# Performance work log

Hardware: AMD Instinct MI355X
Metric: run time of the kernel (lower is better)

Reference implementation:

```python
import jax, jax.numpy as jnp
import numpy as np

N, B, S, A = 4, 32768, 512, 64
H = 256          # hidden_size
NH = 16          # effective number of heads = attend_dim (range(attend_dim) bug in source)
D = 16           # attend_dim = hidden // attend_heads
EPS_BN = 1e-5


def setup_inputs() -> dict:
    key = jax.random.key(0)
    ks = jax.random.split(key, 16)
    sc = 0.05
    return {
        "states": jax.random.normal(ks[0], (N, B, S), dtype=jnp.float32),
        "actions": jax.random.normal(ks[1], (N, B, A), dtype=jnp.float32),
        # per-agent state+action encoder (enc_fc1)
        "Wenc": jax.random.normal(ks[2], (N, S + A, H), dtype=jnp.float32) * sc,
        "benc": jax.random.normal(ks[3], (N, H), dtype=jnp.float32) * sc,
        # per-agent state encoder (s_enc_fc1)
        "Ws": jax.random.normal(ks[4], (N, S, H), dtype=jnp.float32) * sc,
        "bs": jax.random.normal(ks[5], (N, H), dtype=jnp.float32) * sc,
        # shared per-head extractors (no bias on key/selector; bias on value)
        "Wk": jax.random.normal(ks[6], (NH, H, D), dtype=jnp.float32) * sc,
        "Wsel": jax.random.normal(ks[7], (NH, H, D), dtype=jnp.float32) * sc,
        "Wv": jax.random.normal(ks[8], (NH, H, D), dtype=jnp.float32) * sc,
        "bv": jax.random.normal(ks[9], (NH, D), dtype=jnp.float32) * sc,
        # per-agent critic MLP (input = H + NH*D = 2H)
        "Wc1": jax.random.normal(ks[10], (N, 2 * H, H), dtype=jnp.float32) * sc,
        "bc1": jax.random.normal(ks[11], (N, H), dtype=jnp.float32) * sc,
        "Wc2": jax.random.normal(ks[12], (N, H, A), dtype=jnp.float32) * sc,
        "bc2": jax.random.normal(ks[13], (N, A), dtype=jnp.float32) * sc,
    }


def _lrelu(x):
    return jax.nn.leaky_relu(x, 0.01)


def _bn(x):
    # BatchNorm1d(affine=False), training mode: biased batch stats over batch axis
    m = x.mean(axis=1, keepdims=True)
    v = x.var(axis=1, keepdims=True)
    return (x - m) * jax.lax.rsqrt(v + EPS_BN)


def reference(states, actions, Wenc, benc, Ws, bs, Wk, Wsel, Wv, bv, Wc1, bc1, Wc2, bc2):
    n, b = states.shape[0], states.shape[1]
    # state+action encodings per agent: [n, B, H]
    sa = jnp.concatenate([states, actions], axis=-1)
    sa_enc = _lrelu(jnp.einsum('nbi,nih->nbh', _bn(sa), Wenc) + benc[:, None, :])
    # state encodings per agent: [n, B, H]
    s_enc = _lrelu(jnp.einsum('nbs,nsh->nbh', _bn(states), Ws) + bs[:, None, :])
    # per-head keys/values/selectors: [NH, n, B, D]
    keys = jnp.einsum('nbh,ehd->enbd', sa_enc, Wk)
    vals = _lrelu(jnp.einsum('nbh,ehd->enbd', sa_enc, Wv) + bv[:, None, None, :])
    sel = jnp.einsum('nbh,ehd->enbd', s_enc, Wsel)
    # attention of agent i over agents j != i (self excluded via -inf mask)
    logits = jnp.einsum('eibd,ejbd->eibj', sel, keys) / jnp.sqrt(jnp.float32(D))
    self_mask = jnp.eye(n, dtype=bool)[None, :, None, :]  # [1, i, 1, j]
    probs = jax.nn.softmax(jnp.where(self_mask, -1e9, logits), axis=-1)
    # weighted values: [n, B, NH, D] (head-major concat order)
    other = jnp.einsum('eibj,ejbd->ibed', probs, vals)
    critic_in = jnp.concatenate([s_enc, other.reshape(n, b, NH * D)], axis=-1)  # [n, B, 2H]
    h = _lrelu(jnp.einsum('nbc,nch->nbh', critic_in, Wc1) + bc1[:, None, :])
    all_q = jnp.einsum('nbh,nha->nba', h, Wc2) + bc2[:, None, :]  # [n, B, A]
    idx = jnp.argmax(actions, axis=-1)  # [n, B]
    q = jnp.take_along_axis(all_q, idx[..., None], axis=-1)  # [n, B, 1]
    return q
```

## Files before the change

kernel.cpp:

```cpp
#include <hip/hip_runtime.h>
#include <hip/hip_bf16.h>
#include <cstdint>
#include <cstddef>

using bf16 = __hip_bfloat16;
typedef __attribute__((ext_vector_type(8))) short bf16x8v;
typedef __attribute__((ext_vector_type(4))) float f32x4v;

constexpr int Nn = 4;
constexpr int Bb = 32768;
constexpr int Ss = 512;
constexpr int Av = 64;
constexpr int SA = 576;
constexpr float BN_EPS = 1e-5f;

__device__ __forceinline__ float lrelu(float v){ return v >= 0.f ? v : 0.01f * v; }
__device__ __forceinline__ float bf2f(bf16 x){ return __bfloat162float(x); }
__device__ __forceinline__ short f2bf(float v){
  union { bf16 b; short s; } u; u.b = __float2bfloat16(v); return u.s;
}

__global__ __launch_bounds__(256) void bn_stats(const float* __restrict__ states,
                                                const float* __restrict__ actions,
                                                float* __restrict__ ssum,
                                                float* __restrict__ ssq){
  const int n = blockIdx.z;
  const int f = blockIdx.x * 64 + threadIdx.x;
  const int ty = threadIdx.y;
  const float* p; int step;
  if (f < Ss){ p = states  + (size_t)n*Bb*Ss + f;        step = Ss; }
  else       { p = actions + (size_t)n*Bb*Av + (f - Ss); step = Av; }
  float s = 0.f, q = 0.f;
  const int b0 = blockIdx.y * 512 + ty, bend = blockIdx.y * 512 + 512;
  for (int b = b0; b < bend; b += 4){
    float v = p[(size_t)b * step];
    s += v; q += v * v;
  }
  __shared__ float rs[4][64], rq[4][64];
  rs[ty][threadIdx.x] = s; rq[ty][threadIdx.x] = q;
  __syncthreads();
  if (ty == 0){
    s = rs[0][threadIdx.x] + rs[1][threadIdx.x] + rs[2][threadIdx.x] + rs[3][threadIdx.x];
    q = rq[0][threadIdx.x] + rq[1][threadIdx.x] + rq[2][threadIdx.x] + rq[3][threadIdx.x];
    atomicAdd(&ssum[n*SA + f], s);
    atomicAdd(&ssq [n*SA + f], q);
  }
}

__global__ void bn_finalize(const float* __restrict__ ssum, const float* __restrict__ ssq,
                            float* __restrict__ mean, float* __restrict__ rstd){
  int i = blockIdx.x * 256 + threadIdx.x;
  float m = ssum[i] * (1.f / Bb);
  float v = ssq[i] * (1.f / Bb) - m * m;
  v = fmaxf(v, 0.f);
  mean[i] = m;
  rstd[i] = rsqrtf(v + BN_EPS);
}

__global__ void bias_copy(const float* __restrict__ b1, const float* __restrict__ b2,
                          float* __restrict__ o1, float* __restrict__ o2){
  int i = blockIdx.x * 256 + threadIdx.x;
  if (i < Nn*256){ o1[i] = b1[i]; o2[i] = b2[i]; }
}

template<int HEAD>
__global__ __launch_bounds__(256) void foldT2(const float* __restrict__ src,
                                              const float* __restrict__ scale,
                                              const float* __restrict__ mean,
                                              float* __restrict__ bias_out,
                                              short* __restrict__ dst,
                                              int K, int N){
  const int a  = blockIdx.z;
  const int tx = threadIdx.x & 63;
  const int ty = threadIdx.x >> 6;
  const int f0 = blockIdx.x * 64 + ty * 16;
  const int c  = blockIdx.y * 64 + tx;
  const float* s = src + (HEAD ? 0 : (size_t)a*K*N);
  short tmp[16] __attribute__((aligned(16)));
  float bsum = 0.f;
  #pragma unroll
  for (int j = 0; j < 16; j++){
    const int f = f0 + j;
    float w = HEAD ? s[(((size_t)(c >> 4))*K + f)*16 + (c & 15)]
                   : s[(size_t)f*N + c];
    if (scale) w *= scale[a*SA + f];
    if (mean)  bsum += mean[a*SA + f] * w;
    tmp[j] = f2bf(w);
  }
  short* d = dst + (HEAD ? 0 : (size_t)a*K*N) + (size_t)c*K + f0;
  *(bf16x8v*)d       = *(bf16x8v*)tmp;
  *(bf16x8v*)(d + 8) = *(bf16x8v*)(tmp + 8);
  if (mean){
    __shared__ float red[4][64];
    red[ty][tx] = bsum;
    __syncthreads();
    if (threadIdx.x < 64){
      float t = red[0][threadIdx.x] + red[1][threadIdx.x]
              + red[2][threadIdx.x] + red[3][threadIdx.x];
      atomicAdd(&bias_out[a*N + blockIdx.y*64 + threadIdx.x], -t);
    }
  }
}

template<int BM,int BN,int WM,int WN,int K,int ASRC,bool ACT,bool OUTF32>
__global__ __launch_bounds__(256) void mgemm(const void* A1, const void* A2,
                                             const short* __restrict__ Wp, int wPerAgent,
                                             const float* __restrict__ bias, int biasStride,
                                             void* Out, int outPitch){
  __shared__ __align__(16) short As[BM*40];
  __shared__ __align__(16) short Bs[BN*40];
  const int tid  = threadIdx.x;
  const int a    = blockIdx.z;
  const int row0 = blockIdx.x * BM;
  const int col0 = blockIdx.y * BN;
  const short* Wb = Wp + (size_t)a * wPerAgent;
  constexpr int FM = BM/WM/16, FN = BN/WN/16;
  const int wid = tid >> 6, lane = tid & 63;
  const int wm = wid % WM, wn = wid / WM;
  const int rowB = wm*(BM/WM), colB = wn*(BN/WN);
  const int lrow = lane & 15, lq = lane >> 4;

  f32x4v acc[FM][FN];
  #pragma unroll
  for (int i = 0; i < FM; i++)
    #pragma unroll
    for (int j = 0; j < FN; j++) acc[i][j] = (f32x4v){0.f,0.f,0.f,0.f};

  for (int k0 = 0; k0 < K; k0 += 32){
    {
      constexpr int EA = BM/8;
      int r, kq;
      if constexpr (BM == 128){ r = tid >> 1; kq = (tid & 1)*16; }
      else                    { r = tid >> 2; kq = (tid & 3)*8;  }
      const size_t grow = (size_t)a*Bb + row0 + r;
      #pragma unroll
      for (int c8 = 0; c8 < EA; c8 += 8){
        const int f = k0 + kq + c8;
        if constexpr (ASRC == 0 || ASRC == 1){
          const float* sp;
          if constexpr (ASRC == 0)
            sp = (f < 512) ? (const float*)A1 + grow*512 + f
                           : (const float*)A2 + grow*64 + (f - 512);
          else
            sp = (const float*)A1 + grow*512 + f;
          float4 x0 = *(const float4*)sp;
          float4 x1 = *(const float4*)(sp + 4);
          short tmp[8] = { f2bf(x0.x), f2bf(x0.y), f2bf(x0.z), f2bf(x0.w),
                           f2bf(x1.x), f2bf(x1.y), f2bf(x1.z), f2bf(x1.w) };
          *(bf16x8v*)&As[r*40 + kq + c8] = *(bf16x8v*)tmp;
        } else {
          const short* sp;
          if constexpr (ASRC == 3)
            sp = (f < 256) ? (const short*)A1 + grow*256 + f
                           : (const short*)A2 + grow*256 + (f - 256);
          else
            sp = (const short*)A1 + grow*256 + f;
          *(bf16x8v*)&As[r*40 + kq + c8] = *(const bf16x8v*)sp;
        }
      }
    }
    {
      int n, kq, reps;
      if constexpr      (BN == 256){ n = tid;      kq = 0;            reps = 4; }
      else if constexpr (BN == 128){ n = tid >> 1; kq = (tid & 1)*16; reps = 2; }
      else                         { n = tid >> 2; kq = (tid & 3)*8;  reps = 1; }
      const short* wp = Wb + (size_t)(col0 + n)*K + k0 + kq;
      #pragma unroll
      for (int t = 0; t < reps; t++)
        *(bf16x8v*)&Bs[n*40 + kq + t*8] = *(const bf16x8v*)(wp + t*8);
    }
    __syncthreads();
    bf16x8v af[FM], bfr[FN];
    #pragma unroll
    for (int mi = 0; mi < FM; mi++)
      af[mi] = *(const bf16x8v*)&As[(rowB + mi*16 + lrow)*40 + lq*8];
    #pragma unroll
    for (int ni = 0; ni < FN; ni++)
      bfr[ni] = *(const bf16x8v*)&Bs[(colB + ni*16 + lrow)*40 + lq*8];
    #pragma unroll
    for (int mi = 0; mi < FM; mi++)
      #pragma unroll
      for (int ni = 0; ni < FN; ni++)
        acc[mi][ni] = __builtin_amdgcn_mfma_f32_16x16x32_bf16(af[mi], bfr[ni], acc[mi][ni], 0, 0, 0);
    __syncthreads();
  }
  #pragma unroll
  for (int mi = 0; mi < FM; mi++){
    const size_t gr = (size_t)a*Bb + row0 + rowB + mi*16 + lq*4;
    #pragma unroll
    for (int ni = 0; ni < FN; ni++){
      const int gc = col0 + colB + ni*16 + lrow;
      const float bb = bias ? bias[a*biasStride + gc] : 0.f;
      #pragma unroll
      for (int r = 0; r < 4; r++){
        float v = acc[mi][ni][r] + bb;
        if (ACT) v = lrelu(v);
        if constexpr (OUTF32) ((float*)Out)[(gr + r)*(size_t)outPitch + gc] = v;
        else                  ((bf16*) Out)[(gr + r)*(size_t)outPitch + gc] = __float2bfloat16(v);
      }
    }
  }
}

union B8g { uint4 u; bf16 h[8]; };
__global__ __launch_bounds__(256) void attn_g(const bf16* __restrict__ K_,
                                              const bf16* __restrict__ V_,
                                              bf16* SO){
  const int t = blockIdx.x * 256 + threadIdx.x;
  const int e = t & 15;
  const size_t b = t >> 4;
  const size_t ofs = b*256 + e*16;
  float S[4][16], Kf[4][16], Vf[4][16];
  #pragma unroll
  for (int i = 0; i < 4; i++){
    B8g u0, u1;
    const bf16* sp = SO + (size_t)i*Bb*256 + ofs;
    u0.u = *(const uint4*)sp; u1.u = *(const uint4*)(sp + 8);
    #pragma unroll
    for (int l = 0; l < 8; l++){ S[i][l] = bf2f(u0.h[l]); S[i][8+l] = bf2f(u1.h[l]); }
    const bf16* kp = K_ + (size_t)i*Bb*256 + ofs;
    u0.u = *(const uint4*)kp; u1.u = *(const uint4*)(kp + 8);
    #pragma unroll
    for (int l = 0; l < 8; l++){ Kf[i][l] = bf2f(u0.h[l]); Kf[i][8+l] = bf2f(u1.h[l]); }
    const bf16* vp = V_ + (size_t)i*Bb*256 + ofs;
    u0.u = *(const uint4*)vp; u1.u = *(const uint4*)(vp + 8);
    #pragma unroll
    for (int l = 0; l < 8; l++){ Vf[i][l] = bf2f(u0.h[l]); Vf[i][8+l] = bf2f(u1.h[l]); }
  }
  #pragma unroll
  for (int i = 0; i < 4; i++){
    float lg[4];
    #pragma unroll
    for (int j = 0; j < 4; j++){
      float d = 0.f;
      #pragma unroll
      for (int l = 0; l < 16; l++) d += S[i][l] * Kf[j][l];
      lg[j] = d * 0.25f;
    }
    lg[i] = -1e9f;
    float m = fmaxf(fmaxf(lg[0], lg[1]), fmaxf(lg[2], lg[3]));
    float p[4], s = 0.f;
    #pragma unroll
    for (int j = 0; j < 4; j++){ p[j] = expf(lg[j] - m); s += p[j]; }
    p[i] = 0.f;
    const float inv = 1.f / s;
    float o[16] = {};
    #pragma unroll
    for (int j = 0; j < 4; j++){
      const float pj = p[j] * inv;
      #pragma unroll
      for (int l = 0; l < 16; l++) o[l] += pj * Vf[j][l];
    }
    B8g w0, w1;
    #pragma unroll
    for (int l = 0; l < 8; l++){ w0.h[l] = __float2bfloat16(o[l]); w1.h[l] = __float2bfloat16(o[8+l]); }
    bf16* op = SO + (size_t)i*Bb*256 + ofs;
    *(uint4*)op       = w0.u;
    *(uint4*)(op + 8) = w1.u;
  }
}

__global__ __launch_bounds__(256) void sel_q(const float* __restrict__ actions,
                                             const float* __restrict__ allq,
                                             float* __restrict__ out){
  const size_t i = (size_t)blockIdx.x * 256 + threadIdx.x;
  const float* ap = actions + i*64;
  float best = ap[0]; int bi = 0;
  for (int j = 1; j < 64; j++){
    float v = ap[j];
    if (v > best){ best = v; bi = j; }
  }
  out[i] = allq[i*64 + bi];
}

constexpr int RB = 4;

template<int K>
__device__ __forceinline__ void gemm4_glb(const float* __restrict__ st,
                                          const float* __restrict__ ac,
                                          const float* __restrict__ mean,
                                          const float* __restrict__ rstd,
                                          int a, int brow0, int tid,
                                          const float* __restrict__ W,
                                          const float* __restrict__ bias, bool act,
                                          float (*Xs)[68], float (*Wt)[264],
                                          float (*Sout)[256]){
  const int r = tid >> 6, c4 = (tid & 63) * 4;
  float acc[4] = {};
  for (int k0 = 0; k0 < K; k0 += 8){
    if (tid < 32){
      const int rb = tid >> 3, kq = tid & 7;
      const int f = k0 + kq;
      float v = (f < Ss) ? st[((size_t)a*Bb + brow0 + rb)*Ss + f]
                         : ac[((size_t)a*Bb + brow0 + rb)*Av + (f - Ss)];
      Xs[kq][rb] = (v - mean[a*SA + f]) * rstd[a*SA + f];
    }
    {
      const int wk = tid >> 5, wc = (tid & 31) * 8;
      const float* wp = W + (size_t)(k0 + wk) * 256 + wc;
      *(float4*)&Wt[wk][wc]     = *(const float4*)wp;
      *(float4*)&Wt[wk][wc + 4] = *(const float4*)(wp + 4);
    }
    __syncthreads();
    #pragma unroll
    for (int kk = 0; kk < 8; kk++){
      const float av = Xs[kk][r];
      float4 w = *(const float4*)&Wt[kk][c4];
      acc[0] += av*w.x; acc[1] += av*w.y; acc[2] += av*w.z; acc[3] += av*w.w;
    }
    __syncthreads();
  }
  float4 o;
  o.x = acc[0] + (bias ? bias[c4+0] : 0.f);
  o.y = acc[1] + (bias ? bias[c4+1] : 0.f);
  o.z = acc[2] + (bias ? bias[c4+2] : 0.f);
  o.w = acc[3] + (bias ? bias[c4+3] : 0.f);
  if (act){ o.x = lrelu(o.x); o.y = lrelu(o.y); o.z = lrelu(o.z); o.w = lrelu(o.w); }
  *(float4*)&Sout[a*RB + r][c4] = o;
}

template<int K, bool HEAD>
__device__ __forceinline__ void gemm4_lds(const float (*S1)[256], const float (*S2)[256],
                                          int a, int tid,
                                          const float* __restrict__ W,
                                          const float* __restrict__ bias, bool act,
                                          float (*Wt)[264], float (*Sout)[256]){
  const int r = tid >> 6, c4 = (tid & 63) * 4;
  float acc[4] = {};
  for (int k0 = 0; k0 < K; k0 += 8){
    if (HEAD){
      const int wk = tid >> 5, c8 = (tid & 31) * 8;
      const int e = c8 >> 4, d0 = c8 & 15;
      const float* wp = W + (size_t)e*(256*16) + (size_t)(k0 + wk)*16 + d0;
      *(float4*)&Wt[wk][c8]     = *(const float4*)wp;
      *(float4*)&Wt[wk][c8 + 4] = *(const float4*)(wp + 4);
    } else {
      const int wk = tid >> 5, wc = (tid & 31) * 8;
      const float* wp = W + (size_t)(k0 + wk)*256 + wc;
      *(float4*)&Wt[wk][wc]     = *(const float4*)wp;
      *(float4*)&Wt[wk][wc + 4] = *(const float4*)(wp + 4);
    }
    __syncthreads();
    const float (*src)[256] = (k0 < 256) ? S1 : S2;
    const int kb = (k0 < 256) ? k0 : k0 - 256;
    const float* arow = &src[a*RB + r][kb];
    #pragma unroll
    for (int kk = 0; kk < 8; kk++){
      const float av = arow[kk];
      float4 w = *(const float4*)&Wt[kk][c4];
      acc[0] += av*w.x; acc[1] += av*w.y; acc[2] += av*w.z; acc[3] += av*w.w;
    }
    __syncthreads();
  }
  float4 o;
  o.x = acc[0] + (bias ? bias[c4+0] : 0.f);
  o.y = acc[1] + (bias ? bias[c4+1] : 0.f);
  o.z = acc[2] + (bias ? bias[c4+2] : 0.f);
  o.w = acc[3] + (bias ? bias[c4+3] : 0.f);
  if (act){ o.x = lrelu(o.x); o.y = lrelu(o.y); o.z = lrelu(o.z); o.w = lrelu(o.w); }
  *(float4*)&Sout[a*RB + r][c4] = o;
}

__global__ __launch_bounds__(256) void fused(
    const float* __restrict__ states, const float* __restrict__ actions,
    const float* __restrict__ mean,  const float* __restrict__ rstd,
    const float* __restrict__ Wenc, const float* __restrict__ benc,
    const float* __restrict__ Wsx,  const float* __restrict__ bsx,
    const float* __restrict__ Wk,   const float* __restrict__ Wsel,
    const float* __restrict__ Wv,   const float* __restrict__ bv,
    const float* __restrict__ Wc1,  const float* __restrict__ bc1,
    const float* __restrict__ Wc2,  const float* __restrict__ bc2,
    float* __restrict__ qout){
  __shared__ float A [16][256];
  __shared__ float Bs2[16][256];
  __shared__ float C [16][256];
  __shared__ float Wt[8][264];
  __shared__ float Xs[8][68];
  __shared__ float Cq[4][68];
  const int tid   = threadIdx.x;
  const int brow0 = blockIdx.x * RB;
  for (int a = 0; a < Nn; a++)
    gemm4_glb<Ss>(states, actions, mean, rstd, a, brow0, tid,
                  Wsx + (size_t)a*Ss*256, bsx + a*256, true, Xs, Wt, A);
  __syncthreads();
  for (int a = 0; a < Nn; a++)
    gemm4_lds<256, true>(A, nullptr, a, tid, Wsel, nullptr, false, Wt, C);
  __syncthreads();
  for (int a = 0; a < Nn; a++)
    gemm4_glb<SA>(states, actions, mean, rstd, a, brow0, tid,
                  Wenc + (size_t)a*SA*256, benc + a*256, true, Xs, Wt, A);
  __syncthreads();
  for (int a = 0; a < Nn; a++)
    gemm4_lds<256, true>(A, nullptr, a, tid, Wk, nullptr, false, Wt, Bs2);
  __syncthreads();
  for (int a = 0; a < Nn; a++)
    gemm4_lds<256, true>(A, nullptr, a, tid, Wv, bv, true, Wt, A);
  __syncthreads();
  if (tid < 64){
    const int rb = tid >> 4, e = tid & 15;
    const int co = e * 16;
    float S[4][16], Kf[4][16], Vf[4][16];
    #pragma unroll
    for (int i = 0; i < 4; i++)
      #pragma unroll
      for (int l = 0; l < 16; l++){
        S[i][l]  = C  [i*RB + rb][co + l];
        Kf[i][l] = Bs2[i*RB + rb][co + l];
        Vf[i][l] = A  [i*RB + rb][co + l];
      }
    #pragma unroll
    for (int i = 0; i < 4; i++){
      float lg[4];
      #pragma unroll
      for (int j = 0; j < 4; j++){
        float d = 0.f;
        #pragma unroll
        for (int l = 0; l < 16; l++) d += S[i][l] * Kf[j][l];
        lg[j] = d * 0.25f;
      }
      lg[i] = -1e9f;
      float m = fmaxf(fmaxf(lg[0], lg[1]), fmaxf(lg[2], lg[3]));
      float p[4], s = 0.f;
      #pragma unroll
      for (int j = 0; j < 4; j++){ p[j] = expf(lg[j] - m); s += p[j]; }
      p[i] = 0.f;
      const float inv = 1.f / s;
      float o[16] = {};
      #pragma unroll
      for (int j = 0; j < 4; j++){
        const float pj = p[j] * inv;
        #pragma unroll
        for (int l = 0; l < 16; l++) o[l] += pj * Vf[j][l];
      }
      #pragma unroll
      for (int l = 0; l < 16; l++) C[i*RB + rb][co + l] = o[l];
    }
  }
  __syncthreads();
  for (int a = 0; a < Nn; a++)
    gemm4_glb<Ss>(states, actions, mean, rstd, a, brow0, tid,
                  Wsx + (size_t)a*Ss*256, bsx + a*256, true, Xs, Wt, A);
  __syncthreads();
  for (int a = 0; a < Nn; a++)
    gemm4_lds<512, false>(A, C, a, tid, Wc1 + (size_t)a*512*256, bc1 + a*256, true, Wt, Bs2);
  __syncthreads();
  for (int a = 0; a < Nn; a++){
    const int r2 = tid >> 6, c2 = tid & 63;
    float acc = 0.f;
    for (int k0 = 0; k0 < 256; k0 += 8){
      const int wk = tid >> 5, wc = (tid & 31) * 2;
      const float* wp = Wc2 + (size_t)a*256*64 + (size_t)(k0 + wk)*64 + wc;
      Wt[wk][wc]     = wp[0];
      Wt[wk][wc + 1] = wp[1];
      __syncthreads();
      #pragma unroll
      for (int kk = 0; kk < 8; kk++) acc += Bs2[a*RB + r2][k0 + kk] * Wt[kk][c2];
      __syncthreads();
    }
    Cq[r2][c2] = acc + bc2[a*64 + c2];
    __syncthreads();
    if (tid < RB){
      const float* ap = actions + ((size_t)a*Bb + brow0 + tid)*Av;
      float best = ap[0]; int bi = 0;
      for (int j = 1; j < Av; j++){
        float v = ap[j];
        if (v > best){ best = v; bi = j; }
      }
      qout[(size_t)a*Bb + brow0 + tid] = Cq[tid][bi];
    }
    __syncthreads();
  }
}

extern "C" void kernel_launch(void* const* d_in, const int* in_sizes, int n_in,
                              void* d_out, int out_size, void* d_ws, size_t ws_size,
                              hipStream_t stream){
  (void)in_sizes; (void)n_in; (void)out_size;
  const float* states  = (const float*)d_in[0];
  const float* actions = (const float*)d_in[1];
  const float* Wenc    = (const float*)d_in[2];
  const float* benc    = (const float*)d_in[3];
  const float* Wsx     = (const float*)d_in[4];
  const float* bsx     = (const float*)d_in[5];
  const float* Wk      = (const float*)d_in[6];
  const float* Wsel    = (const float*)d_in[7];
  const float* Wv      = (const float*)d_in[8];
  const float* bv      = (const float*)d_in[9];
  const float* Wc1     = (const float*)d_in[10];
  const float* bc1     = (const float*)d_in[11];
  const float* Wc2     = (const float*)d_in[12];
  const float* bc2     = (const float*)d_in[13];
  float* qout = (float*)d_out;

  char* base = (char*)d_ws;
  float* ssum = (float*)base;
  float* ssq  = ssum + Nn*SA;
  float* mean = ssq  + Nn*SA;
  float* rstd = mean + Nn*SA;
  size_t off = 4*Nn*SA*sizeof(float);
  float* benc_p = (float*)(base + off); off += 4096;
  float* bs_p   = (float*)(base + off); off += 4096;
  short* Wenc_p = (short*)(base + off); off += (size_t)Nn*SA*256*2;
  short* Ws_p   = (short*)(base + off); off += (size_t)Nn*Ss*256*2;
  short* Whk_p  = (short*)(base + off); off += 256*256*2;
  short* Whs_p  = (short*)(base + off); off += 256*256*2;
  short* Whv_p  = (short*)(base + off); off += 256*256*2;
  short* Wc1_p  = (short*)(base + off); off += (size_t)Nn*512*256*2;
  short* Wc2_p  = (short*)(base + off); off += (size_t)Nn*64*256*2;
  const size_t BUFB = (size_t)Nn*Bb*256*2;
  bf16* S   = (bf16*)(base + off); off += BUFB;
  bf16* SEL = (bf16*)(base + off); off += BUFB;
  bf16* E   = (bf16*)(base + off); off += BUFB;
  bf16* KB  = (bf16*)(base + off); off += BUFB;
  const size_t need = off;
  float* ALLQ = (float*)E;

  hipMemsetAsync(ssum, 0, 2*Nn*SA*sizeof(float), stream);
  bn_stats<<<dim3(9, 64, Nn), dim3(64, 4), 0, stream>>>(states, actions, ssum, ssq);
  bn_finalize<<<dim3(9), dim3(256), 0, stream>>>(ssum, ssq, mean, rstd);

  if (ws_size >= need){
    bias_copy<<<dim3(4), 256, 0, stream>>>(benc, bsx, benc_p, bs_p);
    foldT2<0><<<dim3(SA/64, 4, Nn), 256, 0, stream>>>(Wenc, rstd, mean, benc_p, Wenc_p, SA, 256);
    foldT2<0><<<dim3(Ss/64, 4, Nn), 256, 0, stream>>>(Wsx,  rstd, mean, bs_p,   Ws_p,  Ss, 256);
    foldT2<1><<<dim3(4, 4, 1), 256, 0, stream>>>(Wk,   nullptr, nullptr, nullptr, Whk_p, 256, 256);
    foldT2<1><<<dim3(4, 4, 1), 256, 0, stream>>>(Wsel, nullptr, nullptr, nullptr, Whs_p, 256, 256);
    foldT2<1><<<dim3(4, 4, 1), 256, 0, stream>>>(Wv,   nullptr, nullptr, nullptr, Whv_p, 256, 256);
    foldT2<0><<<dim3(8, 4, Nn), 256, 0, stream>>>(Wc1, nullptr, nullptr, nullptr, Wc1_p, 512, 256);
    foldT2<0><<<dim3(4, 1, Nn), 256, 0, stream>>>(Wc2, nullptr, nullptr, nullptr, Wc2_p, 256, 64);

    mgemm<128,128,2,2,576,0,true,false><<<dim3(Bb/128, 2, Nn), 256, 0, stream>>>(
        states, actions, Wenc_p, SA*256, benc_p, 256, E, 256);
    mgemm<128,128,2,2,512,1,true,false><<<dim3(Bb/128, 2, Nn), 256, 0, stream>>>(
        states, nullptr, Ws_p, Ss*256, bs_p, 256, S, 256);
    mgemm<128,128,2,2,256,2,false,false><<<dim3(Bb/128, 2, Nn), 256, 0, stream>>>(
        S, nullptr, Whs_p, 0, nullptr, 0, SEL, 256);
    mgemm<128,128,2,2,256,2,false,false><<<dim3(Bb/128, 2, Nn), 256, 0, stream>>>(
        E, nullptr, Whk_p, 0, nullptr, 0, KB, 256);
    mgemm<64,256,1,4,256,2,true,false><<<dim3(Bb/64, 1, Nn), 256, 0, stream>>>(
        E, nullptr, Whv_p, 0, bv, 0, E, 256);
    attn_g<<<dim3(Bb*16/256), 256, 0, stream>>>(KB, E, SEL);
    mgemm<128,128,2,2,512,3,true,false><<<dim3(Bb/128, 2, Nn), 256, 0, stream>>>(
        S, SEL, Wc1_p, 512*256, bc1, 256, KB, 256);
    mgemm<128,64,2,2,256,2,false,true><<<dim3(Bb/128, 1, Nn), 256, 0, stream>>>(
        KB, nullptr, Wc2_p, 64*256, bc2, 64, ALLQ, 64);
    sel_q<<<dim3(Nn*Bb/256), 256, 0, stream>>>(actions, ALLQ, qout);
  } else {
    fused<<<dim3(Bb/RB), 256, 0, stream>>>(states, actions, mean, rstd,
                                           Wenc, benc, Wsx, bsx,
                                           Wk, Wsel, Wv, bv,
                                           Wc1, bc1, Wc2, bc2, qout);
  }
}
```

Baseline: 1.016 ms.

## Fuse bf16 input conversion into BN stats pass and retile GEMMs to 64x256

The batch-norm statistics kernel now reads four features per thread with float4 loads and also writes a bf16 copy of the concatenated states and actions into a workspace buffer. The two encoder GEMMs then read that bf16 buffer instead of re-reading and converting the fp32 inputs twice, and most GEMMs switch from 128x128 to 64x256 tiles. The SEL and KB buffers are aliased onto the Xbf region, which is only safe because Xbf is dead by the time they are written. The trade-off is an extra bf16 write of the inputs in exchange for halving fp32 input reads and the repeated conversion work.

New measurement: 1.046 ms. 3.0% more time.

```diff
diff --git a/kernel.cpp b/kernel.cpp
--- a/kernel.cpp
+++ b/kernel.cpp
@@ -5,6 +5,7 @@
 
 using bf16 = __hip_bfloat16;
 typedef __attribute__((ext_vector_type(8))) short bf16x8v;
+typedef __attribute__((ext_vector_type(4))) short bf16x4v;
 typedef __attribute__((ext_vector_type(4))) float f32x4v;
 
 constexpr int Nn = 4;
@@ -20,30 +21,51 @@
   union { bf16 b; short s; } u; u.b = __float2bfloat16(v); return u.s;
 }
 
-__global__ __launch_bounds__(256) void bn_stats(const float* __restrict__ states,
-                                                const float* __restrict__ actions,
-                                                float* __restrict__ ssum,
-                                                float* __restrict__ ssq){
-  const int n = blockIdx.z;
-  const int f = blockIdx.x * 64 + threadIdx.x;
+template<bool WRX>
+__global__ __launch_bounds__(256) void conv_stats(const float* __restrict__ states,
+                                                  const float* __restrict__ actions,
+                                                  float* __restrict__ ssum,
+                                                  float* __restrict__ ssq,
+                                                  short* __restrict__ Xbf){
+  const int n  = blockIdx.z;
+  const int tx = threadIdx.x;
   const int ty = threadIdx.y;
-  const float* p; int step;
-  if (f < Ss){ p = states  + (size_t)n*Bb*Ss + f;        step = Ss; }
-  else       { p = actions + (size_t)n*Bb*Av + (f - Ss); step = Av; }
-  float s = 0.f, q = 0.f;
+  const int g  = blockIdx.x * 64 + tx;
+  const bool on = g < (SA / 4);
+  const int f  = g * 4;
+  const float* p = nullptr; int step = 0;
+  if (on){
+    if (f < Ss){ p = states  + (size_t)n*Bb*Ss + f;        step = Ss; }
+    else       { p = actions + (size_t)n*Bb*Av + (f - Ss); step = Av; }
+  }
+  float s0=0.f,s1=0.f,s2=0.f,s3=0.f,q0=0.f,q1=0.f,q2=0.f,q3=0.f;
   const int b0 = blockIdx.y * 512 + ty, bend = blockIdx.y * 512 + 512;
-  for (int b = b0; b < bend; b += 4){
-    float v = p[(size_t)b * step];
-    s += v; q += v * v;
-  }
-  __shared__ float rs[4][64], rq[4][64];
-  rs[ty][threadIdx.x] = s; rq[ty][threadIdx.x] = q;
-  __syncthreads();
-  if (ty == 0){
-    s = rs[0][threadIdx.x] + rs[1][threadIdx.x] + rs[2][threadIdx.x] + rs[3][threadIdx.x];
-    q = rq[0][threadIdx.x] + rq[1][threadIdx.x] + rq[2][threadIdx.x] + rq[3][threadIdx.x];
-    atomicAdd(&ssum[n*SA + f], s);
-    atomicAdd(&ssq [n*SA + f], q);
+  if (on){
+    for (int b = b0; b < bend; b += 4){
+      float4 v = *(const float4*)(p + (size_t)b*step);
+      if (WRX){
+        short t4[4] __attribute__((aligned(8))) =
+            { f2bf(v.x), f2bf(v.y), f2bf(v.z), f2bf(v.w) };
+        *(bf16x4v*)&Xbf[((size_t)n*Bb + b)*SA + f] = *(bf16x4v*)t4;
+      }
+      s0 += v.x; q0 += v.x*v.x;
+      s1 += v.y; q1 += v.y*v.y;
+      s2 += v.z; q2 += v.z*v.z;
+      s3 += v.w; q3 += v.w*v.w;
+    }
+  }
+  __shared__ float rs[4][64][4], rq[4][64][4];
+  rs[ty][tx][0]=s0; rs[ty][tx][1]=s1; rs[ty][tx][2]=s2; rs[ty][tx][3]=s3;
+  rq[ty][tx][0]=q0; rq[ty][tx][1]=q1; rq[ty][tx][2]=q2; rq[ty][tx][3]=q3;
+  __syncthreads();
+  if (ty == 0 && on){
+    #pragma unroll
+    for (int j = 0; j < 4; j++){
+      float ts = rs[0][tx][j]+rs[1][tx][j]+rs[2][tx][j]+rs[3][tx][j];
+      float tq = rq[0][tx][j]+rq[1][tx][j]+rq[2][tx][j]+rq[3][tx][j];
+      atomicAdd(&ssum[n*SA + f + j], ts);
+      atomicAdd(&ssq [n*SA + f + j], tq);
+    }
   }
 }
 
@@ -102,7 +124,7 @@
   }
 }
 
-template<int BM,int BN,int WM,int WN,int K,int ASRC,bool ACT,bool OUTF32>
+template<int BM,int BN,int WM,int WN,int K,int ASRC,int AP,bool ACT,bool OUTF32>
 __global__ __launch_bounds__(256) void mgemm(const void* A1, const void* A2,
                                              const short* __restrict__ Wp, int wPerAgent,
                                              const float* __restrict__ bias, int biasStride,
@@ -154,7 +176,7 @@
             sp = (f < 256) ? (const short*)A1 + grow*256 + f
                            : (const short*)A2 + grow*256 + (f - 256);
           else
-            sp = (const short*)A1 + grow*256 + f;
+            sp = (const short*)A1 + grow*(size_t)AP + f;
           *(bf16x8v*)&As[r*40 + kq + c8] = *(const bf16x8v*)sp;
         }
       }
@@ -508,18 +530,22 @@
   short* Wc1_p  = (short*)(base + off); off += (size_t)Nn*512*256*2;
   short* Wc2_p  = (short*)(base + off); off += (size_t)Nn*64*256*2;
   const size_t BUFB = (size_t)Nn*Bb*256*2;
-  bf16* S   = (bf16*)(base + off); off += BUFB;
-  bf16* SEL = (bf16*)(base + off); off += BUFB;
-  bf16* E   = (bf16*)(base + off); off += BUFB;
-  bf16* KB  = (bf16*)(base + off); off += BUFB;
+  const size_t XBFB = (size_t)Nn*Bb*SA*2;
+  short* Xbf = (short*)(base + off);
+  bf16* SEL  = (bf16*)(base + off);
+  bf16* KB   = (bf16*)(base + off + BUFB);
+  off += XBFB;
+  bf16* S    = (bf16*)(base + off); off += BUFB;
+  bf16* E    = (bf16*)(base + off); off += BUFB;
   const size_t need = off;
   float* ALLQ = (float*)E;
 
   hipMemsetAsync(ssum, 0, 2*Nn*SA*sizeof(float), stream);
-  bn_stats<<<dim3(9, 64, Nn), dim3(64, 4), 0, stream>>>(states, actions, ssum, ssq);
-  bn_finalize<<<dim3(9), dim3(256), 0, stream>>>(ssum, ssq, mean, rstd);
 
   if (ws_size >= need){
+    conv_stats<true><<<dim3(3, 64, Nn), dim3(64, 4), 0, stream>>>(states, actions, ssum, ssq, Xbf);
+    bn_finalize<<<dim3(9), dim3(256), 0, stream>>>(ssum, ssq, mean, rstd);
+
     bias_copy<<<dim3(4), 256, 0, stream>>>(benc, bsx, benc_p, bs_p);
     foldT2<0><<<dim3(SA/64, 4, Nn), 256, 0, stream>>>(Wenc, rstd, mean, benc_p, Wenc_p, SA, 256);
     foldT2<0><<<dim3(Ss/64, 4, Nn), 256, 0, stream>>>(Wsx,  rstd, mean, bs_p,   Ws_p,  Ss, 256);
@@ -529,23 +555,25 @@
     foldT2<0><<<dim3(8, 4, Nn), 256, 0, stream>>>(Wc1, nullptr, nullptr, nullptr, Wc1_p, 512, 256);
     foldT2<0><<<dim3(4, 1, Nn), 256, 0, stream>>>(Wc2, nullptr, nullptr, nullptr, Wc2_p, 256, 64);
 
-    mgemm<128,128,2,2,576,0,true,false><<<dim3(Bb/128, 2, Nn), 256, 0, stream>>>(
-        states, actions, Wenc_p, SA*256, benc_p, 256, E, 256);
-    mgemm<128,128,2,2,512,1,true,false><<<dim3(Bb/128, 2, Nn), 256, 0, stream>>>(
-        states, nullptr, Ws_p, Ss*256, bs_p, 256, S, 256);
-    mgemm<128,128,2,2,256,2,false,false><<<dim3(Bb/128, 2, Nn), 256, 0, stream>>>(
+    mgemm<64,256,1,4,576,2,SA,true,false><<<dim3(Bb/64, 1, Nn), 256, 0, stream>>>(
+        Xbf, nullptr, Wenc_p, SA*256, benc_p, 256, E, 256);
+    mgemm<64,256,1,4,512,2,SA,true,false><<<dim3(Bb/64, 1, Nn), 256, 0, stream>>>(
+        Xbf, nullptr, Ws_p, Ss*256, bs_p, 256, S, 256);
+    mgemm<64,256,1,4,256,2,256,false,false><<<dim3(Bb/64, 1, Nn), 256, 0, stream>>>(
         S, nullptr, Whs_p, 0, nullptr, 0, SEL, 256);
-    mgemm<128,128,2,2,256,2,false,false><<<dim3(Bb/128, 2, Nn), 256, 0, stream>>>(
+    mgemm<64,256,1,4,256,2,256,false,false><<<dim3(Bb/64, 1, Nn), 256, 0, stream>>>(
         E, nullptr, Whk_p, 0, nullptr, 0, KB, 256);
-    mgemm<64,256,1,4,256,2,true,false><<<dim3(Bb/64, 1, Nn), 256, 0, stream>>>(
+    mgemm<64,256,1,4,256,2,256,true,false><<<dim3(Bb/64, 1, Nn), 256, 0, stream>>>(
         E, nullptr, Whv_p, 0, bv, 0, E, 256);
     attn_g<<<dim3(Bb*16/256), 256, 0, stream>>>(KB, E, SEL);
-    mgemm<128,128,2,2,512,3,true,false><<<dim3(Bb/128, 2, Nn), 256, 0, stream>>>(
+    mgemm<64,256,1,4,512,3,256,true,false><<<dim3(Bb/64, 1, Nn), 256, 0, stream>>>(
         S, SEL, Wc1_p, 512*256, bc1, 256, KB, 256);
-    mgemm<128,64,2,2,256,2,false,true><<<dim3(Bb/128, 1, Nn), 256, 0, stream>>>(
+    mgemm<128,64,2,2,256,2,256,false,true><<<dim3(Bb/128, 1, Nn), 256, 0, stream>>>(
         KB, nullptr, Wc2_p, 64*256, bc2, 64, ALLQ, 64);
     sel_q<<<dim3(Nn*Bb/256), 256, 0, stream>>>(actions, ALLQ, qout);
   } else {
+    conv_stats<false><<<dim3(3, 64, Nn), dim3(64, 4), 0, stream>>>(states, actions, ssum, ssq, nullptr);
+    bn_finalize<<<dim3(9), dim3(256), 0, stream>>>(ssum, ssq, mean, rstd);
     fused<<<dim3(Bb/RB), 256, 0, stream>>>(states, actions, mean, rstd,
                                            Wenc, benc, Wsx, bsx,
                                            Wk, Wsel, Wv, bv,
```
